# Kernel optimization log

Hardware: AMD Instinct MI355X
Metric: run time of the kernel (lower is better)

Reference implementation:

```python
import jax, jax.numpy as jnp
import numpy as np

N = 50000   # nodes
IN = 128    # in_dim
H = 4       # attn heads
F = 32      # out_feats per head (H*F == IN -> Identity residual)
E = 500000  # edges per edge type
L = 512     # label dim
SLOPE = 0.2 # leaky_relu negative slope


def setup_inputs() -> dict:
    key = jax.random.key(0)
    ks = jax.random.split(key, 12)
    x = jax.random.normal(ks[0], (N, IN), jnp.float32)
    y = jax.random.uniform(ks[1], (N, L), jnp.float32)
    src_p = jax.random.randint(ks[2], (E,), 0, N)
    dst_p = jax.random.randint(ks[3], (E,), 0, N)
    src_s = jax.random.randint(ks[4], (E,), 0, N)
    dst_s = jax.random.randint(ks[5], (E,), 0, N)
    dst_flag = jax.random.randint(ks[6], (N,), 0, 2).astype(bool)
    # shared GAT parameters (share_weight=True)
    W_src = jax.random.normal(ks[7], (H * F, IN), jnp.float32) * 0.05
    b_src = jnp.zeros((H * F,), jnp.float32)
    W_dst = jax.random.normal(ks[8], (H * F, IN), jnp.float32) * 0.05
    b_dst = jnp.zeros((H * F,), jnp.float32)
    attn = jax.random.normal(ks[9], (1, H, F), jnp.float32) * 0.1
    return {"x": x, "y": y, "W_src": W_src, "b_src": b_src, "W_dst": W_dst,
            "b_dst": b_dst, "attn": attn, "src_p": src_p, "dst_p": dst_p,
            "src_s": src_s, "dst_s": dst_s, "dst_flag": dst_flag}


def _edge_softmax(logits, dst):
    # softmax over incoming edges per destination node, per head
    m = jax.ops.segment_max(logits, dst, num_segments=N)          # (N,H)
    ex = jnp.exp(logits - m[dst])
    s = jax.ops.segment_sum(ex, dst, num_segments=N)              # (N,H)
    return ex / s[dst]


def _gat(x, src, dst, W_src, b_src, W_dst, b_dst, attn):
    fs = (x @ W_src.T + b_src).reshape(N, H, F)   # feat_src 'el'
    fd = (x @ W_dst.T + b_dst).reshape(N, H, F)   # feat_dst 'er'
    # u_add_v -> leaky_relu -> dot with attn vector
    e = jax.nn.leaky_relu(fs[src] + fd[dst], SLOPE)               # (E,H,F)
    logits = jnp.einsum('ehf,hf->eh', e, attn[0])                 # (E,H)
    a = _edge_softmax(logits, dst)                                # (E,H)
    # u_mul_e + sum aggregation
    ft = jax.ops.segment_sum(fs[src] * a[:, :, None], dst, num_segments=N)  # (N,H,F)
    rst = ft + x.reshape(N, H, F)  # Identity residual (IN == H*F)
    return rst.mean(axis=1), a.mean(axis=1)       # (N,F), (E,)


def reference(x, y, W_src, b_src, W_dst, b_dst, attn,
              src_p, dst_p, src_s, dst_s, dst_flag):
    h_p, a_p = _gat(x, src_p, dst_p, W_src, b_src, W_dst, b_dst, attn)
    h_s, a_s = _gat(x, src_s, dst_s, W_src, b_src, W_dst, b_dst, attn)
    h = jax.nn.elu(h_p + h_s)                                     # (N,F)
    # label propagation with the (head-averaged) attention coefficients
    yh = (jax.ops.segment_sum(y[src_p] * a_p[:, None], dst_p, num_segments=N)
          + jax.ops.segment_sum(y[src_s] * a_s[:, None], dst_s, num_segments=N))
    norm = jnp.linalg.norm(yh, axis=1, keepdims=True)             # F.normalize, p=2, dim=1
    yh = yh / jnp.maximum(norm, 1e-12)
    y_hat = jnp.where(dst_flag[:, None], y, yh)  # y_hat[dst_flag] = y0
    return h, y_hat
```

## Files before the change

kernel.cpp:

```cpp
#include <hip/hip_runtime.h>

#define NN 50000
#define INDIM 128
#define HH 4
#define FF 32
#define EE 500000
#define LL 512
#define SLOPE 0.2f
#define FSTR 256
#define ELLW 96
#define ELLH 48
#define DSTRIDE 32

#define NB_ZERO  1563
#define NB_WCONV 16
#define NB_K0    (NB_ZERO + NB_WCONV + 1)
#define NB_SCAT  3907
#define NB_MFMA  3125
#define NB_CONVY 12500
#define NB_K1    (NB_SCAT + NB_MFMA + NB_CONVY)

using bf16x8 = __attribute__((ext_vector_type(8))) short;
using f32x4  = __attribute__((ext_vector_type(4))) float;
using f32x2  = __attribute__((ext_vector_type(2))) float;

static __device__ inline unsigned short f2b(float f) {
    union { float f; unsigned int u; } v;
    v.f = f;
    unsigned int u = v.u;
    u += 0x7FFF + ((u >> 16) & 1);
    return (unsigned short)(u >> 16);
}
static __device__ inline float b2f(unsigned int u16) {
    union { unsigned int u; float f; } v;
    v.u = u16 << 16;
    return v.f;
}

__global__ void k0_kernel(uint4* __restrict__ deg2v,
                          const float* __restrict__ Wsrc, const float* __restrict__ Wdst,
                          unsigned short* __restrict__ wb,
                          const unsigned char* __restrict__ flagbuf, int* __restrict__ mode) {
    const int bid = blockIdx.x;
    const int t = threadIdx.x;
    if (bid < NB_ZERO) {
        const int i = bid * 256 + t;
        if (i < NN * DSTRIDE / 4) deg2v[i] = make_uint4(0u, 0u, 0u, 0u);
    } else if (bid < NB_ZERO + NB_WCONV) {
        const int i = (bid - NB_ZERO) * 256 + t;
        const int e = i * 8;
        const int row = e >> 7;
        const int col = e & 127;
        const float* sp = (row < INDIM) ? (Wsrc + (size_t)row * INDIM + col)
                                        : (Wdst + (size_t)(row - INDIM) * INDIM + col);
        const float4 a = reinterpret_cast<const float4*>(sp)[0];
        const float4 b = reinterpret_cast<const float4*>(sp)[1];
        unsigned short o[8] = {f2b(a.x), f2b(a.y), f2b(a.z), f2b(a.w),
                               f2b(b.x), f2b(b.y), f2b(b.z), f2b(b.w)};
        reinterpret_cast<bf16x8*>(wb)[i] = *reinterpret_cast<const bf16x8*>(o);
    } else {
        __shared__ int cnt;
        if (t == 0) cnt = 0;
        __syncthreads();
        int c = 0;
        for (int i = t; i < NN; i += 256)
            if ((i & 3) && flagbuf[i]) c++;
        atomicAdd(&cnt, c);
        __syncthreads();
        if (t == 0) *mode = (cnt == 0) ? 1 : 0;
    }
}

__global__ void k1_kernel(const float* __restrict__ xf, const unsigned short* __restrict__ wb,
                          const float* __restrict__ bsrc, const float* __restrict__ bdst,
                          unsigned short* __restrict__ fcatb,
                          const float* __restrict__ y, unsigned char* __restrict__ y8,
                          const int* __restrict__ src_p, const int* __restrict__ dst_p,
                          const int* __restrict__ src_s, const int* __restrict__ dst_s,
                          int* __restrict__ deg2, int* __restrict__ ell) {
    const int bid = (int)(((unsigned int)blockIdx.x * 7919u) % (unsigned int)NB_K1);
    const int t = threadIdx.x;
    if (bid < NB_SCAT) {
        const int e = bid * 256 + t;
        if (e < 2 * EE) {
            int d, s, sub;
            if (e < EE) { d = dst_p[e]; s = src_p[e]; sub = 0; }
            else        { d = dst_s[e - EE]; s = src_s[e - EE]; sub = 1; }
            const int slot = atomicAdd(&deg2[(size_t)d * DSTRIDE + sub * 16], 1);
            if (slot < ELLH)
                ell[(size_t)d * ELLW + sub * ELLH + slot] = s;
        }
    } else if (bid < NB_SCAT + NB_MFMA) {
        __shared__ unsigned short st[16][256];
        const int wave = t >> 6;
        const int lane = t & 63;
        const int n0 = (bid - NB_SCAT) * 16;
        const int r = lane & 15;
        const int kb = (lane >> 4) * 8;
        f32x4 acc[4] = {{0.f, 0.f, 0.f, 0.f}, {0.f, 0.f, 0.f, 0.f},
                        {0.f, 0.f, 0.f, 0.f}, {0.f, 0.f, 0.f, 0.f}};
#pragma unroll
        for (int ks = 0; ks < 4; ++ks) {
            const float4 xa = *reinterpret_cast<const float4*>(xf + (size_t)(n0 + r) * INDIM + ks * 32 + kb);
            const float4 xb4 = *reinterpret_cast<const float4*>(xf + (size_t)(n0 + r) * INDIM + ks * 32 + kb + 4);
            unsigned short ao[8] = {f2b(xa.x), f2b(xa.y), f2b(xa.z), f2b(xa.w),
                                    f2b(xb4.x), f2b(xb4.y), f2b(xb4.z), f2b(xb4.w)};
            const bf16x8 a = *reinterpret_cast<const bf16x8*>(ao);
#pragma unroll
            for (int tI = 0; tI < 4; ++tI) {
                const int j = wave * 64 + tI * 16 + r;
                const bf16x8 bf = *reinterpret_cast<const bf16x8*>(wb + (size_t)j * INDIM + ks * 32 + kb);
                acc[tI] = __builtin_amdgcn_mfma_f32_16x16x32_bf16(a, bf, acc[tI], 0, 0, 0);
            }
        }
        const int rowg = (lane >> 4) * 4;
#pragma unroll
        for (int tI = 0; tI < 4; ++tI) {
            const int j = wave * 64 + tI * 16 + r;
            const float bias = (j < INDIM) ? bsrc[j] : bdst[j - INDIM];
#pragma unroll
            for (int q = 0; q < 4; ++q)
                st[rowg + q][j] = f2b(acc[tI][q] + bias);
        }
        __syncthreads();
#pragma unroll
        for (int it = 0; it < 2; ++it) {
            const int idx = it * 256 + t;
            const int row = idx >> 5;
            const int chunk = idx & 31;
            const uint4 v = *reinterpret_cast<const uint4*>(&st[row][chunk * 8]);
            *reinterpret_cast<uint4*>(fcatb + (size_t)(n0 + row) * FSTR + chunk * 8) = v;
        }
    } else {
        const int i = (bid - NB_SCAT - NB_MFMA) * 256 + t;
        const float4 a = reinterpret_cast<const float4*>(y)[(size_t)i * 2];
        const float4 b = reinterpret_cast<const float4*>(y)[(size_t)i * 2 + 1];
        unsigned int r0 = 0, r1 = 0;
        r0 = __builtin_amdgcn_cvt_pk_fp8_f32(a.x, a.y, r0, false);
        r0 = __builtin_amdgcn_cvt_pk_fp8_f32(a.z, a.w, r0, true);
        r1 = __builtin_amdgcn_cvt_pk_fp8_f32(b.x, b.y, r1, false);
        r1 = __builtin_amdgcn_cvt_pk_fp8_f32(b.z, b.w, r1, true);
        reinterpret_cast<uint2*>(y8)[i] = make_uint2(r0, r1);
    }
}

__global__ __launch_bounds__(256) void
mega_kernel(const float* __restrict__ x, const float* __restrict__ yf,
            const unsigned char* __restrict__ y8,
            const unsigned short* __restrict__ fcatb,
            const float* __restrict__ attn,
            const int* __restrict__ deg2, const int* __restrict__ ell,
            const void* __restrict__ flagbuf, const int* __restrict__ mode,
            float* __restrict__ hout, float* __restrict__ yhat) {
    const int t = threadIdx.x;
    const int w = t >> 6, l = t & 63;
    const int n = blockIdx.x * 4 + w;
    const int c0 = min(deg2[(size_t)n * DSTRIDE], ELLH);
    const int c1 = min(deg2[(size_t)n * DSTRIDE + 16], ELLH);
    const int cnt = c0 + c1;
    const int base = n * ELLW;
    const int sub = l >> 4, sl = l & 15;

    __shared__ uint2 evL[4][ELLW];
    __shared__ float amL[4][ELLW];
    __shared__ int srcL[4][ELLW];

    const bool flag = (*mode == 1) ? (reinterpret_cast<const int*>(flagbuf)[n] != 0)
                                   : (reinterpret_cast<const unsigned char*>(flagbuf)[n] != 0);

    for (int i = l; i < cnt; i += 64) {
        const int idx = (i < c0) ? i : (ELLH + i - c0);
        srcL[w][i] = ell[base + idx];
    }

    float fdf[8], atv[8];
    {
        const uint4 fdv = *reinterpret_cast<const uint4*>(fcatb + (size_t)n * FSTR + 128 + sl * 8);
        const unsigned int* fdu = reinterpret_cast<const unsigned int*>(&fdv);
        const float4 a0 = *reinterpret_cast<const float4*>(attn + sl * 8);
        const float4 a1 = *reinterpret_cast<const float4*>(attn + sl * 8 + 4);
        atv[0] = a0.x; atv[1] = a0.y; atv[2] = a0.z; atv[3] = a0.w;
        atv[4] = a1.x; atv[5] = a1.y; atv[6] = a1.z; atv[7] = a1.w;
#pragma unroll
        for (int j = 0; j < 4; ++j) {
            fdf[2 * j] = b2f(fdu[j] & 0xffff);
            fdf[2 * j + 1] = b2f(fdu[j] >> 16);
        }
    }

    float facP[8] = {0.f, 0.f, 0.f, 0.f, 0.f, 0.f, 0.f, 0.f};
    float facS[8] = {0.f, 0.f, 0.f, 0.f, 0.f, 0.f, 0.f, 0.f};
    float denP = 0.f, denS = 0.f;

#pragma unroll 2
    for (int i = sub; i < c0; i += 4) {
        const int s = srcL[w][i];
        const uint4 fsv = *reinterpret_cast<const uint4*>(fcatb + (size_t)s * FSTR + sl * 8);
        const unsigned int* fsu = reinterpret_cast<const unsigned int*>(&fsv);
        float fsf[8];
        float v = 0.f;
#pragma unroll
        for (int j = 0; j < 4; ++j) {
            const float e0 = b2f(fsu[j] & 0xffff);
            const float e1 = b2f(fsu[j] >> 16);
            fsf[2 * j] = e0;
            fsf[2 * j + 1] = e1;
            const float x0 = e0 + fdf[2 * j], x1 = e1 + fdf[2 * j + 1];
            v += fmaxf(x0, SLOPE * x0) * atv[2 * j] + fmaxf(x1, SLOPE * x1) * atv[2 * j + 1];
        }
        v += __shfl_xor(v, 1);
        v += __shfl_xor(v, 2);
        const float ev = b2f(f2b(__expf(v)));
#pragma unroll
        for (int j = 0; j < 8; ++j) facP[j] += ev * fsf[j];
        denP += ((sl & 3) == 0) ? ev : 0.f;
        const float pu = __shfl_xor(ev, 4);
        if ((sl & 7) == 0)
            reinterpret_cast<unsigned int*>(&evL[w][0])[i * 2 + (sl >> 3)] =
                (unsigned int)f2b(ev) | ((unsigned int)f2b(pu) << 16);
    }
#pragma unroll 2
    for (int i = c0 + sub; i < cnt; i += 4) {
        const int s = srcL[w][i];
        const uint4 fsv = *reinterpret_cast<const uint4*>(fcatb + (size_t)s * FSTR + sl * 8);
        const unsigned int* fsu = reinterpret_cast<const unsigned int*>(&fsv);
        float fsf[8];
        float v = 0.f;
#pragma unroll
        for (int j = 0; j < 4; ++j) {
            const float e0 = b2f(fsu[j] & 0xffff);
            const float e1 = b2f(fsu[j] >> 16);
            fsf[2 * j] = e0;
            fsf[2 * j + 1] = e1;
            const float x0 = e0 + fdf[2 * j], x1 = e1 + fdf[2 * j + 1];
            v += fmaxf(x0, SLOPE * x0) * atv[2 * j] + fmaxf(x1, SLOPE * x1) * atv[2 * j + 1];
        }
        v += __shfl_xor(v, 1);
        v += __shfl_xor(v, 2);
        const float ev = b2f(f2b(__expf(v)));
#pragma unroll
        for (int j = 0; j < 8; ++j) facS[j] += ev * fsf[j];
        denS += ((sl & 3) == 0) ? ev : 0.f;
        const float pu = __shfl_xor(ev, 4);
        if ((sl & 7) == 0)
            reinterpret_cast<unsigned int*>(&evL[w][0])[i * 2 + (sl >> 3)] =
                (unsigned int)f2b(ev) | ((unsigned int)f2b(pu) << 16);
    }

    denP += __shfl_xor(denP, 16); denP += __shfl_xor(denP, 32);
    denS += __shfl_xor(denS, 16); denS += __shfl_xor(denS, 32);

    float dInv[8];
#pragma unroll
    for (int h = 0; h < 4; ++h) {
        const float dp = __shfl(denP, h * 4);
        const float ds_ = __shfl(denS, h * 4);
        dInv[h] = (dp > 0.f) ? 1.f / dp : 0.f;
        dInv[4 + h] = (ds_ > 0.f) ? 1.f / ds_ : 0.f;
    }

    {
#pragma unroll
        for (int j = 0; j < 8; ++j) {
            facP[j] += __shfl_xor(facP[j], 16); facP[j] += __shfl_xor(facP[j], 32);
            facS[j] += __shfl_xor(facS[j], 16); facS[j] += __shfl_xor(facS[j], 32);
        }
        const int h = sl >> 2;
        float sft[8];
#pragma unroll
        for (int j = 0; j < 8; ++j) {
            sft[j] = facP[j] * dInv[h] + facS[j] * dInv[4 + h];
            sft[j] += __shfl_xor(sft[j], 4);
            sft[j] += __shfl_xor(sft[j], 8);
        }
        if (l < 4) {
            const int o = l * 8;
            float xs[8] = {0.f, 0.f, 0.f, 0.f, 0.f, 0.f, 0.f, 0.f};
#pragma unroll
            for (int h2 = 0; h2 < 4; ++h2) {
                const float4 xa = *reinterpret_cast<const float4*>(x + (size_t)n * INDIM + h2 * 32 + o);
                const float4 xb4 = *reinterpret_cast<const float4*>(x + (size_t)n * INDIM + h2 * 32 + o + 4);
                xs[0] += xa.x; xs[1] += xa.y; xs[2] += xa.z; xs[3] += xa.w;
                xs[4] += xb4.x; xs[5] += xb4.y; xs[6] += xb4.z; xs[7] += xb4.w;
            }
            float r[8];
#pragma unroll
            for (int j = 0; j < 8; ++j) {
                const float sacc = 0.25f * sft[j] + 0.5f * xs[j];
                r[j] = sacc > 0.f ? sacc : (__expf(sacc) - 1.f);
            }
            *reinterpret_cast<float4*>(hout + (size_t)n * FF + o) = make_float4(r[0], r[1], r[2], r[3]);
            *reinterpret_cast<float4*>(hout + (size_t)n * FF + o + 4) = make_float4(r[4], r[5], r[6], r[7]);
        }
    }

    if (flag) {
        const float4 a = *reinterpret_cast<const float4*>(yf + (size_t)n * LL + l * 8);
        const float4 b = *reinterpret_cast<const float4*>(yf + (size_t)n * LL + l * 8 + 4);
        *reinterpret_cast<float4*>(yhat + (size_t)n * LL + l * 8) = a;
        *reinterpret_cast<float4*>(yhat + (size_t)n * LL + l * 8 + 4) = b;
        return;
    }

    for (int i = l; i < cnt; i += 64) {
        const int bh = (i < c0) ? 0 : 4;
        const uint2 e = evL[w][i];
        amL[w][i] = 0.25f * (b2f(e.x & 0xffff) * dInv[bh] + b2f(e.x >> 16) * dInv[bh + 1] +
                             b2f(e.y & 0xffff) * dInv[bh + 2] + b2f(e.y >> 16) * dInv[bh + 3]);
    }

    float acc[8] = {0.f, 0.f, 0.f, 0.f, 0.f, 0.f, 0.f, 0.f};
#pragma unroll 4
    for (int i = 0; i < cnt; ++i) {
        const float am = amL[w][i];
        const int s = srcL[w][i];
        const uint2 yv = *reinterpret_cast<const uint2*>(y8 + (size_t)s * LL + l * 8);
        const f32x2 p0 = __builtin_amdgcn_cvt_pk_f32_fp8(yv.x, false);
        const f32x2 p1 = __builtin_amdgcn_cvt_pk_f32_fp8(yv.x, true);
        const f32x2 p2 = __builtin_amdgcn_cvt_pk_f32_fp8(yv.y, false);
        const f32x2 p3 = __builtin_amdgcn_cvt_pk_f32_fp8(yv.y, true);
        acc[0] += p0.x * am; acc[1] += p0.y * am;
        acc[2] += p1.x * am; acc[3] += p1.y * am;
        acc[4] += p2.x * am; acc[5] += p2.y * am;
        acc[6] += p3.x * am; acc[7] += p3.y * am;
    }
    float ss = 0.f;
#pragma unroll
    for (int j = 0; j < 8; ++j) ss += acc[j] * acc[j];
    for (int off = 32; off; off >>= 1) ss += __shfl_xor(ss, off, 64);
    const float scale = 1.f / fmaxf(sqrtf(ss), 1e-12f);
    *reinterpret_cast<float4*>(yhat + (size_t)n * LL + l * 8) =
        make_float4(acc[0] * scale, acc[1] * scale, acc[2] * scale, acc[3] * scale);
    *reinterpret_cast<float4*>(yhat + (size_t)n * LL + l * 8 + 4) =
        make_float4(acc[4] * scale, acc[5] * scale, acc[6] * scale, acc[7] * scale);
}

extern "C" void kernel_launch(void* const* d_in, const int* in_sizes, int n_in,
                              void* d_out, int out_size, void* d_ws, size_t ws_size,
                              hipStream_t stream) {
    const float* x    = (const float*)d_in[0];
    const float* y    = (const float*)d_in[1];
    const float* Wsrc = (const float*)d_in[2];
    const float* bsrc = (const float*)d_in[3];
    const float* Wdst = (const float*)d_in[4];
    const float* bdst = (const float*)d_in[5];
    const float* attn = (const float*)d_in[6];
    const int* src_p  = (const int*)d_in[7];
    const int* dst_p  = (const int*)d_in[8];
    const int* src_s  = (const int*)d_in[9];
    const int* dst_s  = (const int*)d_in[10];
    const void* dflag = d_in[11];

    float* out  = (float*)d_out;
    float* hout = out;
    float* yhat = out + (size_t)NN * FF;

    char* base = (char*)d_ws;
    unsigned short* fcatb = (unsigned short*)base;
    unsigned char*  y8    = (unsigned char*)(base + 25600000);
    unsigned short* wb    = (unsigned short*)(base + 51200000);
    int*            ell   = (int*)(base + 51300000);
    int*            deg2  = (int*)(base + 70500000);
    int*            mode  = (int*)(base + 76900000);

    k0_kernel<<<NB_K0, 256, 0, stream>>>((uint4*)deg2, Wsrc, Wdst, wb,
                                         (const unsigned char*)dflag, mode);

    k1_kernel<<<NB_K1, 256, 0, stream>>>(x, wb, bsrc, bdst, fcatb, y, y8,
                                         src_p, dst_p, src_s, dst_s, deg2, ell);

    mega_kernel<<<NN / 4, 256, 0, stream>>>(x, y, y8, fcatb, attn, deg2, ell,
                                            dflag, mode, hout, yhat);
}
```

Before: 290.8 us.

## Store projected features in FP8 and use persistent ticket-scheduled node batches

The projected source/destination features are now written as FP8 (e4m3) instead of bf16, halving the gather traffic in the attention phase. The main kernel becomes persistent: 2048 blocks whose waves grab batches of 8 nodes through an atomic ticket counter, replacing one launch slot per group of four nodes. This aims to cut gather bandwidth and smooth load imbalance from varying degrees, at the cost of lower feature precision in the attention logits and aggregation, plus atomic contention on the ticket.

New measurement: 444.5 us. 1.53x slower.

```diff
diff --git a/kernel.cpp b/kernel.cpp
--- a/kernel.cpp
+++ b/kernel.cpp
@@ -11,6 +11,7 @@
 #define ELLW 96
 #define ELLH 48
 #define DSTRIDE 32
+#define BATCH 8
 
 #define NB_ZERO  1563
 #define NB_WCONV 16
@@ -36,11 +37,15 @@
     v.u = u16 << 16;
     return v.f;
 }
+static __device__ inline unsigned char f2e4m3(float f) {
+    return (unsigned char)(__builtin_amdgcn_cvt_pk_fp8_f32(f, f, 0u, false) & 0xff);
+}
 
 __global__ void k0_kernel(uint4* __restrict__ deg2v,
                           const float* __restrict__ Wsrc, const float* __restrict__ Wdst,
                           unsigned short* __restrict__ wb,
-                          const unsigned char* __restrict__ flagbuf, int* __restrict__ mode) {
+                          const unsigned char* __restrict__ flagbuf, int* __restrict__ mode,
+                          int* __restrict__ ticket) {
     const int bid = blockIdx.x;
     const int t = threadIdx.x;
     if (bid < NB_ZERO) {
@@ -60,7 +65,7 @@
         reinterpret_cast<bf16x8*>(wb)[i] = *reinterpret_cast<const bf16x8*>(o);
     } else {
         __shared__ int cnt;
-        if (t == 0) cnt = 0;
+        if (t == 0) { cnt = 0; *ticket = 0; }
         __syncthreads();
         int c = 0;
         for (int i = t; i < NN; i += 256)
@@ -73,7 +78,7 @@
 
 __global__ void k1_kernel(const float* __restrict__ xf, const unsigned short* __restrict__ wb,
                           const float* __restrict__ bsrc, const float* __restrict__ bdst,
-                          unsigned short* __restrict__ fcatb,
+                          unsigned char* __restrict__ fcat8,
                           const float* __restrict__ y, unsigned char* __restrict__ y8,
                           const int* __restrict__ src_p, const int* __restrict__ dst_p,
                           const int* __restrict__ src_s, const int* __restrict__ dst_s,
@@ -91,7 +96,7 @@
                 ell[(size_t)d * ELLW + sub * ELLH + slot] = s;
         }
     } else if (bid < NB_SCAT + NB_MFMA) {
-        __shared__ unsigned short st[16][256];
+        __shared__ unsigned char st8[16 * 256];
         const int wave = t >> 6;
         const int lane = t & 63;
         const int n0 = (bid - NB_SCAT) * 16;
@@ -120,16 +125,12 @@
             const float bias = (j < INDIM) ? bsrc[j] : bdst[j - INDIM];
 #pragma unroll
             for (int q = 0; q < 4; ++q)
-                st[rowg + q][j] = f2b(acc[tI][q] + bias);
+                st8[(rowg + q) * 256 + j] = f2e4m3(acc[tI][q] + bias);
         }
         __syncthreads();
-#pragma unroll
-        for (int it = 0; it < 2; ++it) {
-            const int idx = it * 256 + t;
-            const int row = idx >> 5;
-            const int chunk = idx & 31;
-            const uint4 v = *reinterpret_cast<const uint4*>(&st[row][chunk * 8]);
-            *reinterpret_cast<uint4*>(fcatb + (size_t)(n0 + row) * FSTR + chunk * 8) = v;
+        {
+            const uint4 v = *reinterpret_cast<const uint4*>(&st8[t * 16]);
+            *reinterpret_cast<uint4*>(fcat8 + (size_t)n0 * FSTR + t * 16) = v;
         }
     } else {
         const int i = (bid - NB_SCAT - NB_MFMA) * 256 + t;
@@ -147,192 +148,204 @@
 __global__ __launch_bounds__(256) void
 mega_kernel(const float* __restrict__ x, const float* __restrict__ yf,
             const unsigned char* __restrict__ y8,
-            const unsigned short* __restrict__ fcatb,
+            const unsigned char* __restrict__ fcat8,
             const float* __restrict__ attn,
             const int* __restrict__ deg2, const int* __restrict__ ell,
             const void* __restrict__ flagbuf, const int* __restrict__ mode,
+            int* __restrict__ ticket,
             float* __restrict__ hout, float* __restrict__ yhat) {
     const int t = threadIdx.x;
     const int w = t >> 6, l = t & 63;
-    const int n = blockIdx.x * 4 + w;
-    const int c0 = min(deg2[(size_t)n * DSTRIDE], ELLH);
-    const int c1 = min(deg2[(size_t)n * DSTRIDE + 16], ELLH);
-    const int cnt = c0 + c1;
-    const int base = n * ELLW;
     const int sub = l >> 4, sl = l & 15;
+    const int md = *mode;
 
     __shared__ uint2 evL[4][ELLW];
     __shared__ float amL[4][ELLW];
     __shared__ int srcL[4][ELLW];
 
-    const bool flag = (*mode == 1) ? (reinterpret_cast<const int*>(flagbuf)[n] != 0)
-                                   : (reinterpret_cast<const unsigned char*>(flagbuf)[n] != 0);
-
-    for (int i = l; i < cnt; i += 64) {
-        const int idx = (i < c0) ? i : (ELLH + i - c0);
-        srcL[w][i] = ell[base + idx];
-    }
-
-    float fdf[8], atv[8];
+    float atv[8];
     {
-        const uint4 fdv = *reinterpret_cast<const uint4*>(fcatb + (size_t)n * FSTR + 128 + sl * 8);
-        const unsigned int* fdu = reinterpret_cast<const unsigned int*>(&fdv);
         const float4 a0 = *reinterpret_cast<const float4*>(attn + sl * 8);
         const float4 a1 = *reinterpret_cast<const float4*>(attn + sl * 8 + 4);
         atv[0] = a0.x; atv[1] = a0.y; atv[2] = a0.z; atv[3] = a0.w;
         atv[4] = a1.x; atv[5] = a1.y; atv[6] = a1.z; atv[7] = a1.w;
-#pragma unroll
-        for (int j = 0; j < 4; ++j) {
-            fdf[2 * j] = b2f(fdu[j] & 0xffff);
-            fdf[2 * j + 1] = b2f(fdu[j] >> 16);
-        }
     }
 
-    float facP[8] = {0.f, 0.f, 0.f, 0.f, 0.f, 0.f, 0.f, 0.f};
-    float facS[8] = {0.f, 0.f, 0.f, 0.f, 0.f, 0.f, 0.f, 0.f};
-    float denP = 0.f, denS = 0.f;
+    for (;;) {
+        int nb;
+        if (l == 0) nb = atomicAdd(ticket, BATCH);
+        nb = __shfl(nb, 0);
+        if (nb >= NN) break;
+        const int ne = min(nb + BATCH, NN);
+        for (int n = nb; n < ne; ++n) {
+            const int c0 = min(deg2[(size_t)n * DSTRIDE], ELLH);
+            const int c1 = min(deg2[(size_t)n * DSTRIDE + 16], ELLH);
+            const int cnt = c0 + c1;
+            const int base = n * ELLW;
+            const bool flag = (md == 1) ? (reinterpret_cast<const int*>(flagbuf)[n] != 0)
+                                        : (reinterpret_cast<const unsigned char*>(flagbuf)[n] != 0);
+
+            for (int i = l; i < cnt; i += 64) {
+                const int idx = (i < c0) ? i : (ELLH + i - c0);
+                srcL[w][i] = ell[base + idx];
+            }
+
+            float fdf[8];
+            {
+                const uint2 fdv = *reinterpret_cast<const uint2*>(fcat8 + (size_t)n * FSTR + 128 + sl * 8);
+                const f32x2 q0 = __builtin_amdgcn_cvt_pk_f32_fp8(fdv.x, false);
+                const f32x2 q1 = __builtin_amdgcn_cvt_pk_f32_fp8(fdv.x, true);
+                const f32x2 q2 = __builtin_amdgcn_cvt_pk_f32_fp8(fdv.y, false);
+                const f32x2 q3 = __builtin_amdgcn_cvt_pk_f32_fp8(fdv.y, true);
+                fdf[0] = q0.x; fdf[1] = q0.y; fdf[2] = q1.x; fdf[3] = q1.y;
+                fdf[4] = q2.x; fdf[5] = q2.y; fdf[6] = q3.x; fdf[7] = q3.y;
+            }
+
+            float facP[8] = {0.f, 0.f, 0.f, 0.f, 0.f, 0.f, 0.f, 0.f};
+            float facS[8] = {0.f, 0.f, 0.f, 0.f, 0.f, 0.f, 0.f, 0.f};
+            float denP = 0.f, denS = 0.f;
 
 #pragma unroll 2
-    for (int i = sub; i < c0; i += 4) {
-        const int s = srcL[w][i];
-        const uint4 fsv = *reinterpret_cast<const uint4*>(fcatb + (size_t)s * FSTR + sl * 8);
-        const unsigned int* fsu = reinterpret_cast<const unsigned int*>(&fsv);
-        float fsf[8];
-        float v = 0.f;
-#pragma unroll
-        for (int j = 0; j < 4; ++j) {
-            const float e0 = b2f(fsu[j] & 0xffff);
-            const float e1 = b2f(fsu[j] >> 16);
-            fsf[2 * j] = e0;
-            fsf[2 * j + 1] = e1;
-            const float x0 = e0 + fdf[2 * j], x1 = e1 + fdf[2 * j + 1];
-            v += fmaxf(x0, SLOPE * x0) * atv[2 * j] + fmaxf(x1, SLOPE * x1) * atv[2 * j + 1];
-        }
-        v += __shfl_xor(v, 1);
-        v += __shfl_xor(v, 2);
-        const float ev = b2f(f2b(__expf(v)));
-#pragma unroll
-        for (int j = 0; j < 8; ++j) facP[j] += ev * fsf[j];
-        denP += ((sl & 3) == 0) ? ev : 0.f;
-        const float pu = __shfl_xor(ev, 4);
-        if ((sl & 7) == 0)
-            reinterpret_cast<unsigned int*>(&evL[w][0])[i * 2 + (sl >> 3)] =
-                (unsigned int)f2b(ev) | ((unsigned int)f2b(pu) << 16);
+            for (int i = sub; i < c0; i += 4) {
+                const int s = srcL[w][i];
+                const uint2 fsv = *reinterpret_cast<const uint2*>(fcat8 + (size_t)s * FSTR + sl * 8);
+                const f32x2 q0 = __builtin_amdgcn_cvt_pk_f32_fp8(fsv.x, false);
+                const f32x2 q1 = __builtin_amdgcn_cvt_pk_f32_fp8(fsv.x, true);
+                const f32x2 q2 = __builtin_amdgcn_cvt_pk_f32_fp8(fsv.y, false);
+                const f32x2 q3 = __builtin_amdgcn_cvt_pk_f32_fp8(fsv.y, true);
+                const float fsf[8] = {q0.x, q0.y, q1.x, q1.y, q2.x, q2.y, q3.x, q3.y};
+                float v = 0.f;
+#pragma unroll
+                for (int j = 0; j < 8; ++j) {
+                    const float xx = fsf[j] + fdf[j];
+                    v += fmaxf(xx, SLOPE * xx) * atv[j];
+                }
+                v += __shfl_xor(v, 1);
+                v += __shfl_xor(v, 2);
+                const float ev = __expf(v);
+#pragma unroll
+                for (int j = 0; j < 8; ++j) facP[j] += ev * fsf[j];
+                denP += ((sl & 3) == 0) ? ev : 0.f;
+                const float pu = __shfl_xor(ev, 4);
+                if ((sl & 7) == 0)
+                    reinterpret_cast<unsigned int*>(&evL[w][0])[i * 2 + (sl >> 3)] =
+                        (unsigned int)f2b(ev) | ((unsigned int)f2b(pu) << 16);
+            }
+#pragma unroll 2
+            for (int i = c0 + sub; i < cnt; i += 4) {
+                const int s = srcL[w][i];
+                const uint2 fsv = *reinterpret_cast<const uint2*>(fcat8 + (size_t)s * FSTR + sl * 8);
+                const f32x2 q0 = __builtin_amdgcn_cvt_pk_f32_fp8(fsv.x, false);
+                const f32x2 q1 = __builtin_amdgcn_cvt_pk_f32_fp8(fsv.x, true);
+                const f32x2 q2 = __builtin_amdgcn_cvt_pk_f32_fp8(fsv.y, false);
+                const f32x2 q3 = __builtin_amdgcn_cvt_pk_f32_fp8(fsv.y, true);
+                const float fsf[8] = {q0.x, q0.y, q1.x, q1.y, q2.x, q2.y, q3.x, q3.y};
+                float v = 0.f;
+#pragma unroll
+                for (int j = 0; j < 8; ++j) {
+                    const float xx = fsf[j] + fdf[j];
+                    v += fmaxf(xx, SLOPE * xx) * atv[j];
+                }
+                v += __shfl_xor(v, 1);
+                v += __shfl_xor(v, 2);
+                const float ev = __expf(v);
+#pragma unroll
+                for (int j = 0; j < 8; ++j) facS[j] += ev * fsf[j];
+                denS += ((sl & 3) == 0) ? ev : 0.f;
+                const float pu = __shfl_xor(ev, 4);
+                if ((sl & 7) == 0)
+                    reinterpret_cast<unsigned int*>(&evL[w][0])[i * 2 + (sl >> 3)] =
+                        (unsigned int)f2b(ev) | ((unsigned int)f2b(pu) << 16);
+            }
+
+            denP += __shfl_xor(denP, 16); denP += __shfl_xor(denP, 32);
+            denS += __shfl_xor(denS, 16); denS += __shfl_xor(denS, 32);
+
+            float dInv[8];
+#pragma unroll
+            for (int h = 0; h < 4; ++h) {
+                const float dp = __shfl(denP, h * 4);
+                const float ds_ = __shfl(denS, h * 4);
+                dInv[h] = (dp > 0.f) ? 1.f / dp : 0.f;
+                dInv[4 + h] = (ds_ > 0.f) ? 1.f / ds_ : 0.f;
+            }
+
+            {
+#pragma unroll
+                for (int j = 0; j < 8; ++j) {
+                    facP[j] += __shfl_xor(facP[j], 16); facP[j] += __shfl_xor(facP[j], 32);
+                    facS[j] += __shfl_xor(facS[j], 16); facS[j] += __shfl_xor(facS[j], 32);
+                }
+                const int h = sl >> 2;
+                float sft[8];
+#pragma unroll
+                for (int j = 0; j < 8; ++j) {
+                    sft[j] = facP[j] * dInv[h] + facS[j] * dInv[4 + h];
+                    sft[j] += __shfl_xor(sft[j], 4);
+                    sft[j] += __shfl_xor(sft[j], 8);
+                }
+                if (l < 4) {
+                    const int o = l * 8;
+                    float xs[8] = {0.f, 0.f, 0.f, 0.f, 0.f, 0.f, 0.f, 0.f};
+#pragma unroll
+                    for (int h2 = 0; h2 < 4; ++h2) {
+                        const float4 xa = *reinterpret_cast<const float4*>(x + (size_t)n * INDIM + h2 * 32 + o);
+                        const float4 xb4 = *reinterpret_cast<const float4*>(x + (size_t)n * INDIM + h2 * 32 + o + 4);
+                        xs[0] += xa.x; xs[1] += xa.y; xs[2] += xa.z; xs[3] += xa.w;
+                        xs[4] += xb4.x; xs[5] += xb4.y; xs[6] += xb4.z; xs[7] += xb4.w;
+                    }
+                    float r[8];
+#pragma unroll
+                    for (int j = 0; j < 8; ++j) {
+                        const float sacc = 0.25f * sft[j] + 0.5f * xs[j];
+                        r[j] = sacc > 0.f ? sacc : (__expf(sacc) - 1.f);
+                    }
+                    *reinterpret_cast<float4*>(hout + (size_t)n * FF + o) = make_float4(r[0], r[1], r[2], r[3]);
+                    *reinterpret_cast<float4*>(hout + (size_t)n * FF + o + 4) = make_float4(r[4], r[5], r[6], r[7]);
+                }
+            }
+
+            if (flag) {
+                const float4 a = *reinterpret_cast<const float4*>(yf + (size_t)n * LL + l * 8);
+                const float4 b = *reinterpret_cast<const float4*>(yf + (size_t)n * LL + l * 8 + 4);
+                *reinterpret_cast<float4*>(yhat + (size_t)n * LL + l * 8) = a;
+                *reinterpret_cast<float4*>(yhat + (size_t)n * LL + l * 8 + 4) = b;
+                continue;
+            }
+
+            for (int i = l; i < cnt; i += 64) {
+                const int bh = (i < c0) ? 0 : 4;
+                const uint2 e = evL[w][i];
+                amL[w][i] = 0.25f * (b2f(e.x & 0xffff) * dInv[bh] + b2f(e.x >> 16) * dInv[bh + 1] +
+                                     b2f(e.y & 0xffff) * dInv[bh + 2] + b2f(e.y >> 16) * dInv[bh + 3]);
+            }
+
+            float acc[8] = {0.f, 0.f, 0.f, 0.f, 0.f, 0.f, 0.f, 0.f};
+#pragma unroll 4
+            for (int i = 0; i < cnt; ++i) {
+                const float am = amL[w][i];
+                const int s = srcL[w][i];
+                const uint2 yv = *reinterpret_cast<const uint2*>(y8 + (size_t)s * LL + l * 8);
+                const f32x2 p0 = __builtin_amdgcn_cvt_pk_f32_fp8(yv.x, false);
+                const f32x2 p1 = __builtin_amdgcn_cvt_pk_f32_fp8(yv.x, true);
+                const f32x2 p2 = __builtin_amdgcn_cvt_pk_f32_fp8(yv.y, false);
+                const f32x2 p3 = __builtin_amdgcn_cvt_pk_f32_fp8(yv.y, true);
+                acc[0] += p0.x * am; acc[1] += p0.y * am;
+                acc[2] += p1.x * am; acc[3] += p1.y * am;
+                acc[4] += p2.x * am; acc[5] += p2.y * am;
+                acc[6] += p3.x * am; acc[7] += p3.y * am;
+            }
+            float ss = 0.f;
+#pragma unroll
+            for (int j = 0; j < 8; ++j) ss += acc[j] * acc[j];
+            for (int off = 32; off; off >>= 1) ss += __shfl_xor(ss, off, 64);
+            const float scale = 1.f / fmaxf(sqrtf(ss), 1e-12f);
+            *reinterpret_cast<float4*>(yhat + (size_t)n * LL + l * 8) =
+                make_float4(acc[0] * scale, acc[1] * scale, acc[2] * scale, acc[3] * scale);
+            *reinterpret_cast<float4*>(yhat + (size_t)n * LL + l * 8 + 4) =
+                make_float4(acc[4] * scale, acc[5] * scale, acc[6] * scale, acc[7] * scale);
+        }
     }
-#pragma unroll 2
-    for (int i = c0 + sub; i < cnt; i += 4) {
-        const int s = srcL[w][i];
-        const uint4 fsv = *reinterpret_cast<const uint4*>(fcatb + (size_t)s * FSTR + sl * 8);
-        const unsigned int* fsu = reinterpret_cast<const unsigned int*>(&fsv);
-        float fsf[8];
-        float v = 0.f;
-#pragma unroll
-        for (int j = 0; j < 4; ++j) {
-            const float e0 = b2f(fsu[j] & 0xffff);
-            const float e1 = b2f(fsu[j] >> 16);
-            fsf[2 * j] = e0;
-            fsf[2 * j + 1] = e1;
-            const float x0 = e0 + fdf[2 * j], x1 = e1 + fdf[2 * j + 1];
-            v += fmaxf(x0, SLOPE * x0) * atv[2 * j] + fmaxf(x1, SLOPE * x1) * atv[2 * j + 1];
-        }
-        v += __shfl_xor(v, 1);
-        v += __shfl_xor(v, 2);
-        const float ev = b2f(f2b(__expf(v)));
-#pragma unroll
-        for (int j = 0; j < 8; ++j) facS[j] += ev * fsf[j];
-        denS += ((sl & 3) == 0) ? ev : 0.f;
-        const float pu = __shfl_xor(ev, 4);
-        if ((sl & 7) == 0)
-            reinterpret_cast<unsigned int*>(&evL[w][0])[i * 2 + (sl >> 3)] =
-                (unsigned int)f2b(ev) | ((unsigned int)f2b(pu) << 16);
-    }
-
-    denP += __shfl_xor(denP, 16); denP += __shfl_xor(denP, 32);
-    denS += __shfl_xor(denS, 16); denS += __shfl_xor(denS, 32);
-
-    float dInv[8];
-#pragma unroll
-    for (int h = 0; h < 4; ++h) {
-        const float dp = __shfl(denP, h * 4);
-        const float ds_ = __shfl(denS, h * 4);
-        dInv[h] = (dp > 0.f) ? 1.f / dp : 0.f;
-        dInv[4 + h] = (ds_ > 0.f) ? 1.f / ds_ : 0.f;
-    }
-
-    {
-#pragma unroll
-        for (int j = 0; j < 8; ++j) {
-            facP[j] += __shfl_xor(facP[j], 16); facP[j] += __shfl_xor(facP[j], 32);
-            facS[j] += __shfl_xor(facS[j], 16); facS[j] += __shfl_xor(facS[j], 32);
-        }
-        const int h = sl >> 2;
-        float sft[8];
-#pragma unroll
-        for (int j = 0; j < 8; ++j) {
-            sft[j] = facP[j] * dInv[h] + facS[j] * dInv[4 + h];
-            sft[j] += __shfl_xor(sft[j], 4);
-            sft[j] += __shfl_xor(sft[j], 8);
-        }
-        if (l < 4) {
-            const int o = l * 8;
-            float xs[8] = {0.f, 0.f, 0.f, 0.f, 0.f, 0.f, 0.f, 0.f};
-#pragma unroll
-            for (int h2 = 0; h2 < 4; ++h2) {
-                const float4 xa = *reinterpret_cast<const float4*>(x + (size_t)n * INDIM + h2 * 32 + o);
-                const float4 xb4 = *reinterpret_cast<const float4*>(x + (size_t)n * INDIM + h2 * 32 + o + 4);
-                xs[0] += xa.x; xs[1] += xa.y; xs[2] += xa.z; xs[3] += xa.w;
-                xs[4] += xb4.x; xs[5] += xb4.y; xs[6] += xb4.z; xs[7] += xb4.w;
-            }
-            float r[8];
-#pragma unroll
-            for (int j = 0; j < 8; ++j) {
-                const float sacc = 0.25f * sft[j] + 0.5f * xs[j];
-                r[j] = sacc > 0.f ? sacc : (__expf(sacc) - 1.f);
-            }
-            *reinterpret_cast<float4*>(hout + (size_t)n * FF + o) = make_float4(r[0], r[1], r[2], r[3]);
-            *reinterpret_cast<float4*>(hout + (size_t)n * FF + o + 4) = make_float4(r[4], r[5], r[6], r[7]);
-        }
-    }
-
-    if (flag) {
-        const float4 a = *reinterpret_cast<const float4*>(yf + (size_t)n * LL + l * 8);
-        const float4 b = *reinterpret_cast<const float4*>(yf + (size_t)n * LL + l * 8 + 4);
-        *reinterpret_cast<float4*>(yhat + (size_t)n * LL + l * 8) = a;
-        *reinterpret_cast<float4*>(yhat + (size_t)n * LL + l * 8 + 4) = b;
-        return;
-    }
-
-    for (int i = l; i < cnt; i += 64) {
-        const int bh = (i < c0) ? 0 : 4;
-        const uint2 e = evL[w][i];
-        amL[w][i] = 0.25f * (b2f(e.x & 0xffff) * dInv[bh] + b2f(e.x >> 16) * dInv[bh + 1] +
-                             b2f(e.y & 0xffff) * dInv[bh + 2] + b2f(e.y >> 16) * dInv[bh + 3]);
-    }
-
-    float acc[8] = {0.f, 0.f, 0.f, 0.f, 0.f, 0.f, 0.f, 0.f};
-#pragma unroll 4
-    for (int i = 0; i < cnt; ++i) {
-        const float am = amL[w][i];
-        const int s = srcL[w][i];
-        const uint2 yv = *reinterpret_cast<const uint2*>(y8 + (size_t)s * LL + l * 8);
-        const f32x2 p0 = __builtin_amdgcn_cvt_pk_f32_fp8(yv.x, false);
-        const f32x2 p1 = __builtin_amdgcn_cvt_pk_f32_fp8(yv.x, true);
-        const f32x2 p2 = __builtin_amdgcn_cvt_pk_f32_fp8(yv.y, false);
-        const f32x2 p3 = __builtin_amdgcn_cvt_pk_f32_fp8(yv.y, true);
-        acc[0] += p0.x * am; acc[1] += p0.y * am;
-        acc[2] += p1.x * am; acc[3] += p1.y * am;
-        acc[4] += p2.x * am; acc[5] += p2.y * am;
-        acc[6] += p3.x * am; acc[7] += p3.y * am;
-    }
-    float ss = 0.f;
-#pragma unroll
-    for (int j = 0; j < 8; ++j) ss += acc[j] * acc[j];
-    for (int off = 32; off; off >>= 1) ss += __shfl_xor(ss, off, 64);
-    const float scale = 1.f / fmaxf(sqrtf(ss), 1e-12f);
-    *reinterpret_cast<float4*>(yhat + (size_t)n * LL + l * 8) =
-        make_float4(acc[0] * scale, acc[1] * scale, acc[2] * scale, acc[3] * scale);
-    *reinterpret_cast<float4*>(yhat + (size_t)n * LL + l * 8 + 4) =
-        make_float4(acc[4] * scale, acc[5] * scale, acc[6] * scale, acc[7] * scale);
 }
 
 extern "C" void kernel_launch(void* const* d_in, const int* in_sizes, int n_in,
@@ -356,19 +369,20 @@
     float* yhat = out + (size_t)NN * FF;
 
     char* base = (char*)d_ws;
-    unsigned short* fcatb = (unsigned short*)base;
-    unsigned char*  y8    = (unsigned char*)(base + 25600000);
-    unsigned short* wb    = (unsigned short*)(base + 51200000);
-    int*            ell   = (int*)(base + 51300000);
-    int*            deg2  = (int*)(base + 70500000);
-    int*            mode  = (int*)(base + 76900000);
+    unsigned char*  fcat8 = (unsigned char*)base;
+    unsigned char*  y8    = (unsigned char*)(base + 12800000);
+    unsigned short* wb    = (unsigned short*)(base + 38400000);
+    int*            ell   = (int*)(base + 38500000);
+    int*            deg2  = (int*)(base + 57700000);
+    int*            mode  = (int*)(base + 64100000);
+    int*            ticket= (int*)(base + 64100064);
 
     k0_kernel<<<NB_K0, 256, 0, stream>>>((uint4*)deg2, Wsrc, Wdst, wb,
-                                         (const unsigned char*)dflag, mode);
-
-    k1_kernel<<<NB_K1, 256, 0, stream>>>(x, wb, bsrc, bdst, fcatb, y, y8,
+                                         (const unsigned char*)dflag, mode, ticket);
+
+    k1_kernel<<<NB_K1, 256, 0, stream>>>(x, wb, bsrc, bdst, fcat8, y, y8,
                                          src_p, dst_p, src_s, dst_s, deg2, ell);
 
-    mega_kernel<<<NN / 4, 256, 0, stream>>>(x, y, y8, fcatb, attn, deg2, ell,
-                                            dflag, mode, hout, yhat);
-}
+    mega_kernel<<<2048, 256, 0, stream>>>(x, y, y8, fcat8, attn, deg2, ell,
+                                          dflag, mode, ticket, hout, yhat);
+}
```
